# Kernel tuning notes

Measured on AMD Instinct MI355X. Metric: run time of the kernel, lower is better.

The kernel has to match this reference:

```python
import jax, jax.numpy as jnp
import numpy as np

N_NODES = 100000
N_EDGES = 1250000
N_FEAT = 64
HIDDEN = 16
N_CLASSES = 7


def setup_inputs() -> dict:
    key = jax.random.key(0)
    ks = jax.random.split(key, 10)
    x = jax.random.normal(ks[0], (N_NODES, N_FEAT), dtype=jnp.float32)
    edge_index = jax.random.randint(ks[1], (2, N_EDGES), 0, N_NODES, dtype=jnp.int64)
    s = 0.1
    return {
        "x": x,
        "edge_index": edge_index,
        # conv1 MLP: Linear(F,16) ReLU Linear(16,16) ReLU
        "W1": jax.random.normal(ks[2], (N_FEAT, HIDDEN), dtype=jnp.float32) * s,
        "b1": jnp.zeros((HIDDEN,), dtype=jnp.float32),
        "W2": jax.random.normal(ks[3], (HIDDEN, HIDDEN), dtype=jnp.float32) * s,
        "b2": jnp.zeros((HIDDEN,), dtype=jnp.float32),
        # conv2 MLP: Linear(16,16) ReLU Linear(16,C)
        "W3": jax.random.normal(ks[4], (HIDDEN, HIDDEN), dtype=jnp.float32) * s,
        "b3": jnp.zeros((HIDDEN,), dtype=jnp.float32),
        "W4": jax.random.normal(ks[5], (HIDDEN, N_CLASSES), dtype=jnp.float32) * s,
        "b4": jnp.zeros((N_CLASSES,), dtype=jnp.float32),
    }


def _gin_aggregate(h, src, dst):
    # GINConv with default eps=0: (1+eps)*x + sum_{j in N(i)} x_j
    msgs = h[src]  # [E, d] gather
    agg = jax.ops.segment_sum(msgs, dst, num_segments=h.shape[0])  # scatter-add
    return h + agg


def reference(x, edge_index, W1, b1, W2, b2, W3, b3, W4, b4):
    src = edge_index[0]
    dst = edge_index[1]
    # conv1: GIN aggregate + MLP(Linear,ReLU,Linear,ReLU)
    h = _gin_aggregate(x, src, dst)
    h = jax.nn.relu(h @ W1 + b1)
    h = jax.nn.relu(h @ W2 + b2)
    # F.relu after conv1 (idempotent here, kept for faithfulness)
    h = jax.nn.relu(h)
    # conv2: GIN aggregate + MLP(Linear,ReLU,Linear)
    h = _gin_aggregate(h, src, dst)
    h = jax.nn.relu(h @ W3 + b3)
    h = h @ W4 + b4
    return jax.nn.log_softmax(h, axis=1)
```

## Files before the change

### kernel.cpp

```cpp
#include <hip/hip_runtime.h>
#include <math.h>

constexpr int NN = 100000;
constexpr int NE = 1250000;
constexpr int NF = 64;
constexpr int NH = 16;
constexpr int NC = 7;

constexpr int BKT_SHIFT = 7;
constexpr int BKT_NODES = 1 << BKT_SHIFT;
constexpr int NBUCKET = (NN + BKT_NODES - 1) / BKT_NODES;
constexpr int BSTRIDE = 2048;
constexpr int EPB = 4096;
constexpr int NBLK_BUCKET = (NE + EPB - 1) / EPB;
constexpr int CUR_PAD = 16;

__global__ __launch_bounds__(256) void k1_gemm(
    const float* __restrict__ x, const float* __restrict__ W1,
    const float* __restrict__ b1, float* __restrict__ A, float* __restrict__ B,
    int* __restrict__ gcur) {
    int gtid = blockIdx.x * 256 + threadIdx.x;
    if (gtid < NBUCKET * CUR_PAD) gcur[gtid] = 0;

    __shared__ float w[NF * NH];
    __shared__ float bias[NH];
    for (int i = threadIdx.x; i < NF * NH; i += blockDim.x) w[i] = W1[i];
    if (threadIdx.x < NH) bias[threadIdx.x] = b1[threadIdx.x];
    __syncthreads();
    int node = gtid;
    if (node >= NN) return;

    float acc[NH];
#pragma unroll
    for (int j = 0; j < NH; ++j) acc[j] = 0.f;

    const float4* xr = (const float4*)(x + (size_t)node * NF);
#pragma unroll
    for (int k4 = 0; k4 < NF / 4; ++k4) {
        float4 xv = xr[k4];
        int k = k4 * 4;
#pragma unroll
        for (int j = 0; j < NH; ++j) {
            acc[j] += xv.x * w[(k + 0) * NH + j]
                    + xv.y * w[(k + 1) * NH + j]
                    + xv.z * w[(k + 2) * NH + j]
                    + xv.w * w[(k + 3) * NH + j];
        }
    }
    float4* Ar = (float4*)(A + (size_t)node * NH);
    float4* Br = (float4*)(B + (size_t)node * NH);
#pragma unroll
    for (int q = 0; q < NH / 4; ++q) {
        float4 a;
        a.x = acc[q * 4 + 0]; a.y = acc[q * 4 + 1];
        a.z = acc[q * 4 + 2]; a.w = acc[q * 4 + 3];
        Ar[q] = a;
        float4 bv;
        bv.x = a.x + bias[q * 4 + 0]; bv.y = a.y + bias[q * 4 + 1];
        bv.z = a.z + bias[q * 4 + 2]; bv.w = a.w + bias[q * 4 + 3];
        Br[q] = bv;
    }
}

__global__ __launch_bounds__(1024) void k_bucket(
    const int* __restrict__ src, const int* __restrict__ dst,
    int* __restrict__ gcur, unsigned* __restrict__ gbuf) {
    __shared__ int cnt[NBUCKET];
    __shared__ int loff[NBUCKET];
    __shared__ int gb[NBUCKET];
    __shared__ int s[1024];
    __shared__ unsigned sorted[EPB];
    __shared__ unsigned short sortedB[EPB];

    int tid = threadIdx.x;
    for (int i = tid; i < NBUCKET; i += 1024) cnt[i] = 0;
    __syncthreads();

    unsigned pk[4];
    int bk[4];
    int rk[4];
    int base = blockIdx.x * EPB;
    int nval = NE - base; if (nval > EPB) nval = EPB;
#pragma unroll
    for (int k = 0; k < 4; ++k) {
        int e = base + k * 1024 + tid;
        bk[k] = -1;
        if (e < NE) {
            int sv = src[e];
            int d = dst[e];
            int b = d >> BKT_SHIFT;
            bk[k] = b;
            pk[k] = ((unsigned)sv << BKT_SHIFT) | (unsigned)(d & (BKT_NODES - 1));
            rk[k] = atomicAdd(&cnt[b], 1);
        }
    }
    __syncthreads();

    int v = (tid < NBUCKET) ? cnt[tid] : 0;
    s[tid] = v;
    __syncthreads();
    for (int d = 1; d < 1024; d <<= 1) {
        int u = (tid >= d) ? s[tid - d] : 0;
        __syncthreads();
        s[tid] += u;
        __syncthreads();
    }
    if (tid < NBUCKET) {
        loff[tid] = s[tid] - v;
        gb[tid] = (v > 0) ? atomicAdd(&gcur[tid * CUR_PAD], v) : 0;
    }
    __syncthreads();

#pragma unroll
    for (int k = 0; k < 4; ++k) {
        if (bk[k] >= 0) {
            int p = loff[bk[k]] + rk[k];
            sorted[p] = pk[k];
            sortedB[p] = (unsigned short)bk[k];
        }
    }
    __syncthreads();

    for (int i = tid; i < nval; i += 1024) {
        int b = sortedB[i];
        int pos = gb[b] + (i - loff[b]);
        if (pos < BSTRIDE)
            gbuf[(size_t)b * BSTRIDE + pos] = sorted[i];
    }
}

__global__ __launch_bounds__(512) void k_agg1(
    const float* __restrict__ A, float* __restrict__ B, float* __restrict__ A2,
    const int* __restrict__ gcur, unsigned* __restrict__ gbuf,
    unsigned short* __restrict__ soff, unsigned short* __restrict__ scnt,
    const float* __restrict__ W2, const float* __restrict__ b2,
    const float* __restrict__ W3, const float* __restrict__ b3) {
    __shared__ unsigned stage[BSTRIDE];
    __shared__ unsigned eSrc[BSTRIDE];
    __shared__ int cnt[BKT_NODES], off[BKT_NODES], cur[BKT_NODES];
    __shared__ float Bl[BKT_NODES * 17];
    __shared__ float Tl[BKT_NODES * 17];
    __shared__ float w2[NH * NH], w3[NH * NH], bb2[NH], bb3[NH];

    int b = blockIdx.x;
    int tid = threadIdx.x;
    for (int i = tid; i < NH * NH; i += 512) { w2[i] = W2[i]; w3[i] = W3[i]; }
    if (tid < NH) { bb2[tid] = b2[tid]; bb3[tid] = b3[tid]; }
    int n = gcur[b * CUR_PAD];
    if (n > BSTRIDE) n = BSTRIDE;
    if (tid < BKT_NODES) cnt[tid] = 0;
    __syncthreads();

    for (int i = tid; i < n; i += 512) {
        unsigned u = gbuf[(size_t)b * BSTRIDE + i];
        stage[i] = u;
        atomicAdd(&cnt[u & (BKT_NODES - 1)], 1);
    }
    __syncthreads();
    if (tid < BKT_NODES) off[tid] = cnt[tid];
    __syncthreads();
    for (int d = 1; d < BKT_NODES; d <<= 1) {
        int v = 0;
        if (tid < BKT_NODES && tid >= d) v = off[tid - d];
        __syncthreads();
        if (tid < BKT_NODES) off[tid] += v;
        __syncthreads();
    }
    if (tid < BKT_NODES) {
        int st = off[tid] - cnt[tid];
        cur[tid] = st;
        soff[b * BKT_NODES + tid] = (unsigned short)st;
        scnt[b * BKT_NODES + tid] = (unsigned short)cnt[tid];
    }
    __syncthreads();
    for (int i = tid; i < n; i += 512) {
        unsigned u = stage[i];
        int pos = atomicAdd(&cur[u & (BKT_NODES - 1)], 1);
        eSrc[pos] = u >> BKT_SHIFT;
    }
    __syncthreads();

    for (int i = tid; i < n; i += 512) gbuf[(size_t)b * BSTRIDE + i] = eSrc[i];

    int node = tid >> 2;
    int q = (tid & 3) * 4;
    int gnode = (b << BKT_SHIFT) + node;
    int end = off[node];
    int start = end - cnt[node];

    float4 bq = {0.f, 0.f, 0.f, 0.f};
    if (gnode < NN) bq = *(const float4*)(B + (size_t)gnode * NH + q);
    float4 a0 = {0.f, 0.f, 0.f, 0.f}, a1 = {0.f, 0.f, 0.f, 0.f};
    int j = start;
    for (; j + 2 <= end; j += 2) {
        int s0 = eSrc[j];
        int s1 = eSrc[j + 1];
        float4 v0 = *(const float4*)(A + (size_t)s0 * NH + q);
        float4 v1 = *(const float4*)(A + (size_t)s1 * NH + q);
        a0.x += v0.x; a0.y += v0.y; a0.z += v0.z; a0.w += v0.w;
        a1.x += v1.x; a1.y += v1.y; a1.z += v1.z; a1.w += v1.w;
    }
    if (j < end) {
        int s0 = eSrc[j];
        float4 v0 = *(const float4*)(A + (size_t)s0 * NH + q);
        a0.x += v0.x; a0.y += v0.y; a0.z += v0.z; a0.w += v0.w;
    }
    Bl[node * 17 + q + 0] = fmaxf(bq.x + a0.x + a1.x, 0.f);
    Bl[node * 17 + q + 1] = fmaxf(bq.y + a0.y + a1.y, 0.f);
    Bl[node * 17 + q + 2] = fmaxf(bq.z + a0.z + a1.z, 0.f);
    Bl[node * 17 + q + 3] = fmaxf(bq.w + a0.w + a1.w, 0.f);
    __syncthreads();

    float t0 = bb2[q], t1 = bb2[q + 1], t2 = bb2[q + 2], t3 = bb2[q + 3];
#pragma unroll
    for (int k = 0; k < NH; ++k) {
        float hk = Bl[node * 17 + k];
        t0 += hk * w2[k * NH + q + 0];
        t1 += hk * w2[k * NH + q + 1];
        t2 += hk * w2[k * NH + q + 2];
        t3 += hk * w2[k * NH + q + 3];
    }
    Tl[node * 17 + q + 0] = fmaxf(t0, 0.f);
    Tl[node * 17 + q + 1] = fmaxf(t1, 0.f);
    Tl[node * 17 + q + 2] = fmaxf(t2, 0.f);
    Tl[node * 17 + q + 3] = fmaxf(t3, 0.f);
    __syncthreads();

    float z0 = 0.f, z1 = 0.f, z2 = 0.f, z3 = 0.f;
#pragma unroll
    for (int k = 0; k < NH; ++k) {
        float tk = Tl[node * 17 + k];
        z0 += tk * w3[k * NH + q + 0];
        z1 += tk * w3[k * NH + q + 1];
        z2 += tk * w3[k * NH + q + 2];
        z3 += tk * w3[k * NH + q + 3];
    }
    if (gnode < NN) {
        float4 az = {z0, z1, z2, z3};
        *(float4*)(A2 + (size_t)gnode * NH + q) = az;
        float4 bz = {z0 + bb3[q], z1 + bb3[q + 1], z2 + bb3[q + 2], z3 + bb3[q + 3]};
        *(float4*)(B + (size_t)gnode * NH + q) = bz;
    }
}

__global__ __launch_bounds__(512) void k_agg2(
    const float* __restrict__ A2, const float* __restrict__ B,
    const int* __restrict__ gcur, const unsigned* __restrict__ gbuf,
    const unsigned short* __restrict__ soff, const unsigned short* __restrict__ scnt,
    const float* __restrict__ W4, const float* __restrict__ b4,
    float* __restrict__ out) {
    __shared__ unsigned eSrc[BSTRIDE];
    __shared__ int off[BKT_NODES], cnt[BKT_NODES];
    __shared__ float Bl[BKT_NODES * 17];
    __shared__ float w4[NH * NC];
    __shared__ float bb4[NC];

    int b = blockIdx.x;
    int tid = threadIdx.x;
    for (int i = tid; i < NH * NC; i += 512) w4[i] = W4[i];
    if (tid < NC) bb4[tid] = b4[tid];
    int n = gcur[b * CUR_PAD];
    if (n > BSTRIDE) n = BSTRIDE;
    if (tid < BKT_NODES) {
        off[tid] = soff[b * BKT_NODES + tid];
        cnt[tid] = scnt[b * BKT_NODES + tid];
    }
    for (int i = tid; i < n; i += 512) eSrc[i] = gbuf[(size_t)b * BSTRIDE + i];
    __syncthreads();

    int node = tid >> 2;
    int q = (tid & 3) * 4;
    int gnode = (b << BKT_SHIFT) + node;
    int start = off[node];
    int end = start + cnt[node];

    float4 bq = {0.f, 0.f, 0.f, 0.f};
    if (gnode < NN) bq = *(const float4*)(B + (size_t)gnode * NH + q);
    float4 a0 = {0.f, 0.f, 0.f, 0.f}, a1 = {0.f, 0.f, 0.f, 0.f};
    int j = start;
    for (; j + 2 <= end; j += 2) {
        int s0 = eSrc[j];
        int s1 = eSrc[j + 1];
        float4 v0 = *(const float4*)(A2 + (size_t)s0 * NH + q);
        float4 v1 = *(const float4*)(A2 + (size_t)s1 * NH + q);
        a0.x += v0.x; a0.y += v0.y; a0.z += v0.z; a0.w += v0.w;
        a1.x += v1.x; a1.y += v1.y; a1.z += v1.z; a1.w += v1.w;
    }
    if (j < end) {
        int s0 = eSrc[j];
        float4 v0 = *(const float4*)(A2 + (size_t)s0 * NH + q);
        a0.x += v0.x; a0.y += v0.y; a0.z += v0.z; a0.w += v0.w;
    }
    Bl[node * 17 + q + 0] = fmaxf(bq.x + a0.x + a1.x, 0.f);
    Bl[node * 17 + q + 1] = fmaxf(bq.y + a0.y + a1.y, 0.f);
    Bl[node * 17 + q + 2] = fmaxf(bq.z + a0.z + a1.z, 0.f);
    Bl[node * 17 + q + 3] = fmaxf(bq.w + a0.w + a1.w, 0.f);
    __syncthreads();

    if (tid < BKT_NODES) {
        int nd = tid;
        int gn = (b << BKT_SHIFT) + nd;
        if (gn < NN) {
            float o[NC];
#pragma unroll
            for (int c = 0; c < NC; ++c) o[c] = bb4[c];
#pragma unroll
            for (int k = 0; k < NH; ++k) {
                float hk = Bl[nd * 17 + k];
#pragma unroll
                for (int c = 0; c < NC; ++c) o[c] += hk * w4[k * NC + c];
            }
            float m = o[0];
#pragma unroll
            for (int c = 1; c < NC; ++c) m = fmaxf(m, o[c]);
            float s = 0.f;
#pragma unroll
            for (int c = 0; c < NC; ++c) s += expf(o[c] - m);
            float ls = m + logf(s);
            float* op = out + (size_t)gn * NC;
#pragma unroll
            for (int c = 0; c < NC; ++c) op[c] = o[c] - ls;
        }
    }
}

extern "C" void kernel_launch(void* const* d_in, const int* in_sizes, int n_in,
                              void* d_out, int out_size, void* d_ws, size_t ws_size,
                              hipStream_t stream) {
    const float* x  = (const float*)d_in[0];
    const int*   ei = (const int*)d_in[1];
    const float* W1 = (const float*)d_in[2];
    const float* b1 = (const float*)d_in[3];
    const float* W2 = (const float*)d_in[4];
    const float* b2 = (const float*)d_in[5];
    const float* W3 = (const float*)d_in[6];
    const float* b3 = (const float*)d_in[7];
    const float* W4 = (const float*)d_in[8];
    const float* b4 = (const float*)d_in[9];
    float* out = (float*)d_out;

    const int* src = ei;
    const int* dst = ei + NE;

    float*          A    = (float*)d_ws;
    float*          B    = A + (size_t)NN * NH;
    float*          A2   = B + (size_t)NN * NH;
    int*            gcur = (int*)(A2 + (size_t)NN * NH);
    unsigned*       gbuf = (unsigned*)(gcur + NBUCKET * CUR_PAD);
    unsigned short* soff = (unsigned short*)(gbuf + (size_t)NBUCKET * BSTRIDE);
    unsigned short* scnt = soff + (size_t)NBUCKET * BKT_NODES;

    const int nodeBlocks = (NN + 255) / 256;

    k1_gemm<<<nodeBlocks, 256, 0, stream>>>(x, W1, b1, A, B, gcur);
    k_bucket<<<NBLK_BUCKET, 1024, 0, stream>>>(src, dst, gcur, gbuf);
    k_agg1<<<NBUCKET, 512, 0, stream>>>(A, B, A2, gcur, gbuf, soff, scnt, W2, b2, W3, b3);
    k_agg2<<<NBUCKET, 512, 0, stream>>>(A2, B, gcur, gbuf, soff, scnt, W4, b4, out);
}
```

Before: 82.59 us.

## Replace global-atomic bucketing with count, scan, deterministic scatter passes

Edge bucketing moves from per-bucket global atomicAdd on padded cursors to three passes: per-block bucket counts, a per-bucket exclusive scan over blocks, and a scatter that uses the precomputed bases. Edges per block double to 8192. The separate bias-added B buffers are dropped, and biases are added inside the aggregation kernels instead, which cuts global writes and reads. In exchange it adds two kernel launches and a second read of dst, and the bucket layout becomes deterministic.

```diff
diff --git a/kernel.cpp b/kernel.cpp
--- a/kernel.cpp
+++ b/kernel.cpp
@@ -11,23 +11,17 @@
 constexpr int BKT_NODES = 1 << BKT_SHIFT;
 constexpr int NBUCKET = (NN + BKT_NODES - 1) / BKT_NODES;
 constexpr int BSTRIDE = 2048;
-constexpr int EPB = 4096;
+constexpr int EPB = 8192;
 constexpr int NBLK_BUCKET = (NE + EPB - 1) / EPB;
-constexpr int CUR_PAD = 16;
+constexpr int NBLK_PAD = 160;
 
 __global__ __launch_bounds__(256) void k1_gemm(
     const float* __restrict__ x, const float* __restrict__ W1,
-    const float* __restrict__ b1, float* __restrict__ A, float* __restrict__ B,
-    int* __restrict__ gcur) {
-    int gtid = blockIdx.x * 256 + threadIdx.x;
-    if (gtid < NBUCKET * CUR_PAD) gcur[gtid] = 0;
-
+    float* __restrict__ A) {
     __shared__ float w[NF * NH];
-    __shared__ float bias[NH];
     for (int i = threadIdx.x; i < NF * NH; i += blockDim.x) w[i] = W1[i];
-    if (threadIdx.x < NH) bias[threadIdx.x] = b1[threadIdx.x];
-    __syncthreads();
-    int node = gtid;
+    __syncthreads();
+    int node = blockIdx.x * 256 + threadIdx.x;
     if (node >= NN) return;
 
     float acc[NH];
@@ -48,23 +42,53 @@
         }
     }
     float4* Ar = (float4*)(A + (size_t)node * NH);
-    float4* Br = (float4*)(B + (size_t)node * NH);
 #pragma unroll
     for (int q = 0; q < NH / 4; ++q) {
         float4 a;
         a.x = acc[q * 4 + 0]; a.y = acc[q * 4 + 1];
         a.z = acc[q * 4 + 2]; a.w = acc[q * 4 + 3];
         Ar[q] = a;
-        float4 bv;
-        bv.x = a.x + bias[q * 4 + 0]; bv.y = a.y + bias[q * 4 + 1];
-        bv.z = a.z + bias[q * 4 + 2]; bv.w = a.w + bias[q * 4 + 3];
-        Br[q] = bv;
-    }
-}
-
-__global__ __launch_bounds__(1024) void k_bucket(
+    }
+}
+
+__global__ __launch_bounds__(1024) void k_count(
+    const int* __restrict__ dst, int* __restrict__ gcnt) {
+    __shared__ int cnt[NBUCKET];
+    int tid = threadIdx.x;
+    for (int i = tid; i < NBUCKET; i += 1024) cnt[i] = 0;
+    __syncthreads();
+    int base = blockIdx.x * EPB;
+#pragma unroll
+    for (int k = 0; k < 8; ++k) {
+        int e = base + k * 1024 + tid;
+        if (e < NE) atomicAdd(&cnt[dst[e] >> BKT_SHIFT], 1);
+    }
+    __syncthreads();
+    for (int i = tid; i < NBUCKET; i += 1024)
+        gcnt[i * NBLK_PAD + blockIdx.x] = cnt[i];
+}
+
+__global__ __launch_bounds__(256) void k_base(
+    const int* __restrict__ gcnt, int* __restrict__ gbase, int* __restrict__ tcnt) {
+    __shared__ int s[256];
+    int b = blockIdx.x;
+    int tid = threadIdx.x;
+    int v = (tid < NBLK_BUCKET) ? gcnt[b * NBLK_PAD + tid] : 0;
+    s[tid] = v;
+    __syncthreads();
+    for (int d = 1; d < 256; d <<= 1) {
+        int u = (tid >= d) ? s[tid - d] : 0;
+        __syncthreads();
+        s[tid] += u;
+        __syncthreads();
+    }
+    if (tid < NBLK_BUCKET) gbase[b * NBLK_PAD + tid] = s[tid] - v;
+    if (tid == 255) tcnt[b] = s[255];
+}
+
+__global__ __launch_bounds__(1024) void k_scatter(
     const int* __restrict__ src, const int* __restrict__ dst,
-    int* __restrict__ gcur, unsigned* __restrict__ gbuf) {
+    const int* __restrict__ gbase, unsigned* __restrict__ gbuf) {
     __shared__ int cnt[NBUCKET];
     __shared__ int loff[NBUCKET];
     __shared__ int gb[NBUCKET];
@@ -73,16 +97,19 @@
     __shared__ unsigned short sortedB[EPB];
 
     int tid = threadIdx.x;
-    for (int i = tid; i < NBUCKET; i += 1024) cnt[i] = 0;
-    __syncthreads();
-
-    unsigned pk[4];
-    int bk[4];
-    int rk[4];
+    for (int i = tid; i < NBUCKET; i += 1024) {
+        cnt[i] = 0;
+        gb[i] = gbase[i * NBLK_PAD + blockIdx.x];
+    }
+    __syncthreads();
+
+    unsigned pk[8];
+    int bk[8];
+    int rk[8];
     int base = blockIdx.x * EPB;
     int nval = NE - base; if (nval > EPB) nval = EPB;
 #pragma unroll
-    for (int k = 0; k < 4; ++k) {
+    for (int k = 0; k < 8; ++k) {
         int e = base + k * 1024 + tid;
         bk[k] = -1;
         if (e < NE) {
@@ -105,14 +132,11 @@
         s[tid] += u;
         __syncthreads();
     }
-    if (tid < NBUCKET) {
-        loff[tid] = s[tid] - v;
-        gb[tid] = (v > 0) ? atomicAdd(&gcur[tid * CUR_PAD], v) : 0;
-    }
-    __syncthreads();
-
-#pragma unroll
-    for (int k = 0; k < 4; ++k) {
+    if (tid < NBUCKET) loff[tid] = s[tid] - v;
+    __syncthreads();
+
+#pragma unroll
+    for (int k = 0; k < 8; ++k) {
         if (bk[k] >= 0) {
             int p = loff[bk[k]] + rk[k];
             sorted[p] = pk[k];
@@ -130,23 +154,24 @@
 }
 
 __global__ __launch_bounds__(512) void k_agg1(
-    const float* __restrict__ A, float* __restrict__ B, float* __restrict__ A2,
-    const int* __restrict__ gcur, unsigned* __restrict__ gbuf,
+    const float* __restrict__ A, float* __restrict__ A2,
+    const int* __restrict__ tcnt, unsigned* __restrict__ gbuf,
     unsigned short* __restrict__ soff, unsigned short* __restrict__ scnt,
+    const float* __restrict__ b1,
     const float* __restrict__ W2, const float* __restrict__ b2,
-    const float* __restrict__ W3, const float* __restrict__ b3) {
+    const float* __restrict__ W3) {
     __shared__ unsigned stage[BSTRIDE];
     __shared__ unsigned eSrc[BSTRIDE];
     __shared__ int cnt[BKT_NODES], off[BKT_NODES], cur[BKT_NODES];
     __shared__ float Bl[BKT_NODES * 17];
     __shared__ float Tl[BKT_NODES * 17];
-    __shared__ float w2[NH * NH], w3[NH * NH], bb2[NH], bb3[NH];
+    __shared__ float w2[NH * NH], w3[NH * NH], bb1[NH], bb2[NH];
 
     int b = blockIdx.x;
     int tid = threadIdx.x;
     for (int i = tid; i < NH * NH; i += 512) { w2[i] = W2[i]; w3[i] = W3[i]; }
-    if (tid < NH) { bb2[tid] = b2[tid]; bb3[tid] = b3[tid]; }
-    int n = gcur[b * CUR_PAD];
+    if (tid < NH) { bb1[tid] = b1[tid]; bb2[tid] = b2[tid]; }
+    int n = tcnt[b];
     if (n > BSTRIDE) n = BSTRIDE;
     if (tid < BKT_NODES) cnt[tid] = 0;
     __syncthreads();
@@ -189,7 +214,7 @@
     int start = end - cnt[node];
 
     float4 bq = {0.f, 0.f, 0.f, 0.f};
-    if (gnode < NN) bq = *(const float4*)(B + (size_t)gnode * NH + q);
+    if (gnode < NN) bq = *(const float4*)(A + (size_t)gnode * NH + q);
     float4 a0 = {0.f, 0.f, 0.f, 0.f}, a1 = {0.f, 0.f, 0.f, 0.f};
     int j = start;
     for (; j + 2 <= end; j += 2) {
@@ -205,10 +230,10 @@
         float4 v0 = *(const float4*)(A + (size_t)s0 * NH + q);
         a0.x += v0.x; a0.y += v0.y; a0.z += v0.z; a0.w += v0.w;
     }
-    Bl[node * 17 + q + 0] = fmaxf(bq.x + a0.x + a1.x, 0.f);
-    Bl[node * 17 + q + 1] = fmaxf(bq.y + a0.y + a1.y, 0.f);
-    Bl[node * 17 + q + 2] = fmaxf(bq.z + a0.z + a1.z, 0.f);
-    Bl[node * 17 + q + 3] = fmaxf(bq.w + a0.w + a1.w, 0.f);
+    Bl[node * 17 + q + 0] = fmaxf(bq.x + bb1[q + 0] + a0.x + a1.x, 0.f);
+    Bl[node * 17 + q + 1] = fmaxf(bq.y + bb1[q + 1] + a0.y + a1.y, 0.f);
+    Bl[node * 17 + q + 2] = fmaxf(bq.z + bb1[q + 2] + a0.z + a1.z, 0.f);
+    Bl[node * 17 + q + 3] = fmaxf(bq.w + bb1[q + 3] + a0.w + a1.w, 0.f);
     __syncthreads();
 
     float t0 = bb2[q], t1 = bb2[q + 1], t2 = bb2[q + 2], t3 = bb2[q + 3];
@@ -238,28 +263,29 @@
     if (gnode < NN) {
         float4 az = {z0, z1, z2, z3};
         *(float4*)(A2 + (size_t)gnode * NH + q) = az;
-        float4 bz = {z0 + bb3[q], z1 + bb3[q + 1], z2 + bb3[q + 2], z3 + bb3[q + 3]};
-        *(float4*)(B + (size_t)gnode * NH + q) = bz;
     }
 }
 
 __global__ __launch_bounds__(512) void k_agg2(
-    const float* __restrict__ A2, const float* __restrict__ B,
-    const int* __restrict__ gcur, const unsigned* __restrict__ gbuf,
+    const float* __restrict__ A2,
+    const int* __restrict__ tcnt, const unsigned* __restrict__ gbuf,
     const unsigned short* __restrict__ soff, const unsigned short* __restrict__ scnt,
+    const float* __restrict__ b3,
     const float* __restrict__ W4, const float* __restrict__ b4,
     float* __restrict__ out) {
     __shared__ unsigned eSrc[BSTRIDE];
     __shared__ int off[BKT_NODES], cnt[BKT_NODES];
     __shared__ float Bl[BKT_NODES * 17];
     __shared__ float w4[NH * NC];
+    __shared__ float bb3[NH];
     __shared__ float bb4[NC];
 
     int b = blockIdx.x;
     int tid = threadIdx.x;
     for (int i = tid; i < NH * NC; i += 512) w4[i] = W4[i];
+    if (tid < NH) bb3[tid] = b3[tid];
     if (tid < NC) bb4[tid] = b4[tid];
-    int n = gcur[b * CUR_PAD];
+    int n = tcnt[b];
     if (n > BSTRIDE) n = BSTRIDE;
     if (tid < BKT_NODES) {
         off[tid] = soff[b * BKT_NODES + tid];
@@ -275,7 +301,7 @@
     int end = start + cnt[node];
 
     float4 bq = {0.f, 0.f, 0.f, 0.f};
-    if (gnode < NN) bq = *(const float4*)(B + (size_t)gnode * NH + q);
+    if (gnode < NN) bq = *(const float4*)(A2 + (size_t)gnode * NH + q);
     float4 a0 = {0.f, 0.f, 0.f, 0.f}, a1 = {0.f, 0.f, 0.f, 0.f};
     int j = start;
     for (; j + 2 <= end; j += 2) {
@@ -291,10 +317,10 @@
         float4 v0 = *(const float4*)(A2 + (size_t)s0 * NH + q);
         a0.x += v0.x; a0.y += v0.y; a0.z += v0.z; a0.w += v0.w;
     }
-    Bl[node * 17 + q + 0] = fmaxf(bq.x + a0.x + a1.x, 0.f);
-    Bl[node * 17 + q + 1] = fmaxf(bq.y + a0.y + a1.y, 0.f);
-    Bl[node * 17 + q + 2] = fmaxf(bq.z + a0.z + a1.z, 0.f);
-    Bl[node * 17 + q + 3] = fmaxf(bq.w + a0.w + a1.w, 0.f);
+    Bl[node * 17 + q + 0] = fmaxf(bq.x + bb3[q + 0] + a0.x + a1.x, 0.f);
+    Bl[node * 17 + q + 1] = fmaxf(bq.y + bb3[q + 1] + a0.y + a1.y, 0.f);
+    Bl[node * 17 + q + 2] = fmaxf(bq.z + bb3[q + 2] + a0.z + a1.z, 0.f);
+    Bl[node * 17 + q + 3] = fmaxf(bq.w + bb3[q + 3] + a0.w + a1.w, 0.f);
     __syncthreads();
 
     if (tid < BKT_NODES) {
@@ -343,17 +369,20 @@
     const int* dst = ei + NE;
 
     float*          A    = (float*)d_ws;
-    float*          B    = A + (size_t)NN * NH;
-    float*          A2   = B + (size_t)NN * NH;
-    int*            gcur = (int*)(A2 + (size_t)NN * NH);
-    unsigned*       gbuf = (unsigned*)(gcur + NBUCKET * CUR_PAD);
-    unsigned short* soff = (unsigned short*)(gbuf + (size_t)NBUCKET * BSTRIDE);
+    float*          A2   = A + (size_t)NN * NH;
+    unsigned*       gbuf = (unsigned*)(A2 + (size_t)NN * NH);
+    int*            gcnt = (int*)(gbuf + (size_t)NBUCKET * BSTRIDE);
+    int*            gbase= gcnt + (size_t)NBUCKET * NBLK_PAD;
+    int*            tcnt = gbase + (size_t)NBUCKET * NBLK_PAD;
+    unsigned short* soff = (unsigned short*)(tcnt + ((NBUCKET + 3) & ~3));
     unsigned short* scnt = soff + (size_t)NBUCKET * BKT_NODES;
 
     const int nodeBlocks = (NN + 255) / 256;
 
-    k1_gemm<<<nodeBlocks, 256, 0, stream>>>(x, W1, b1, A, B, gcur);
-    k_bucket<<<NBLK_BUCKET, 1024, 0, stream>>>(src, dst, gcur, gbuf);
-    k_agg1<<<NBUCKET, 512, 0, stream>>>(A, B, A2, gcur, gbuf, soff, scnt, W2, b2, W3, b3);
-    k_agg2<<<NBUCKET, 512, 0, stream>>>(A2, B, gcur, gbuf, soff, scnt, W4, b4, out);
-}
+    k1_gemm<<<nodeBlocks, 256, 0, stream>>>(x, W1, A);
+    k_count<<<NBLK_BUCKET, 1024, 0, stream>>>(dst, gcnt);
+    k_base<<<NBUCKET, 256, 0, stream>>>(gcnt, gbase, tcnt);
+    k_scatter<<<NBLK_BUCKET, 1024, 0, stream>>>(src, dst, gbase, gbuf);
+    k_agg1<<<NBUCKET, 512, 0, stream>>>(A, A2, tcnt, gbuf, soff, scnt, b1, W2, b2, W3);
+    k_agg2<<<NBUCKET, 512, 0, stream>>>(A2, tcnt, gbuf, soff, scnt, b3, W4, b4, out);
+}
```

After: 74.76 us. 9.5% less time.
